# Kernel optimization log

Measured on AMD Instinct MI355X. Metric: run time of the kernel, lower is better.

## Reference

```python
import jax, jax.numpy as jnp
import numpy as np

N, E, G = 50000, 150000, 200
D, ED_IN, EH = 320, 15, 32
NB, NT = 3, 9  # conv blocks, edge types


def setup_inputs() -> dict:
    key = jax.random.key(0)
    ks = jax.random.split(key, 16)
    s = 0.02
    return {
        "x": jax.random.normal(ks[0], (N, D), jnp.float32),
        "batch": jnp.sort(jax.random.randint(ks[1], (N,), 0, G)),
        "edge_indices": jax.random.randint(ks[2], (NT, 2, E), 0, N),
        "edge_attrs": jax.random.normal(ks[3], (NT, E, ED_IN), jnp.float32),
        "W1": jax.random.normal(ks[4], (2 * D + ED_IN, EH), jnp.float32) * s,
        "b1": jnp.zeros((EH,), jnp.float32),
        "W2": jax.random.normal(ks[5], (EH, EH), jnp.float32) * s,
        "b2": jnp.zeros((EH,), jnp.float32),
        "Wq": jax.random.normal(ks[6], (NB, NT, D, D), jnp.float32) * s,
        "bq": jnp.zeros((NB, NT, D), jnp.float32),
        "Wk": jax.random.normal(ks[7], (NB, NT, D, D), jnp.float32) * s,
        "bk": jnp.zeros((NB, NT, D), jnp.float32),
        "Wv": jax.random.normal(ks[8], (NB, NT, D, D), jnp.float32) * s,
        "bv": jnp.zeros((NB, NT, D), jnp.float32),
        "We": jax.random.normal(ks[9], (NB, NT, EH, D), jnp.float32) * s,
        "be": jnp.zeros((NB, NT, D), jnp.float32),
        "Ws": jax.random.normal(ks[10], (NB, NT, D, D), jnp.float32) * s,
        "bs": jnp.zeros((NB, NT, D), jnp.float32),
        "gamma": jnp.ones((NB, D), jnp.float32),
        "beta": jnp.zeros((NB, D), jnp.float32),
    }


def _transformer_conv(x, src, dst, ea, Wq, bq, Wk, bk, Wv, bv, We, be, Ws, bs):
    # PyG TransformerConv, heads=1, edge_dim=EH, eval mode (no dropout).
    q = (x @ Wq + bq)[dst]                    # [E, D] query at destination
    e = ea @ We + be                          # [E, D] projected edge attr
    k = (x @ Wk + bk)[src] + e                # [E, D]
    v = (x @ Wv + bv)[src] + e                # [E, D]
    alpha = (q * k).sum(-1) / jnp.sqrt(jnp.float32(D))  # [E]
    amax = jax.ops.segment_max(alpha, dst, num_segments=N)
    amax = jnp.where(jnp.isfinite(amax), amax, 0.0)     # guard empty segments
    ex = jnp.exp(alpha - amax[dst])
    denom = jax.ops.segment_sum(ex, dst, num_segments=N)
    w = ex / (denom[dst] + 1e-16)
    out = jax.ops.segment_sum(w[:, None] * v, dst, num_segments=N)
    return out + x @ Ws + bs                  # root/skip connection


def _graph_layer_norm(x, batch, gamma, beta):
    # PyG gnn.norm.LayerNorm, mode='graph': normalize per graph over nodes+channels.
    cnt = jax.ops.segment_sum(jnp.ones((N,), x.dtype), batch, num_segments=G)
    norm = jnp.maximum(cnt, 1.0) * D          # elements per graph
    mean = jax.ops.segment_sum(x.sum(-1), batch, num_segments=G) / norm
    xc = x - mean[batch][:, None]
    var = jax.ops.segment_sum((xc * xc).sum(-1), batch, num_segments=G) / norm
    out = xc / jnp.sqrt(var + 1e-5)[batch][:, None]
    return out * gamma + beta


def reference(x, batch, edge_indices, edge_attrs, W1, b1, W2, b2,
              Wq, bq, Wk, bk, Wv, bv, We, be, Ws, bs, gamma, beta):
    # Edge MLP preprocessing (uses original node features x).
    new_ea = []
    for t in range(NT):
        src, dst = edge_indices[t, 0], edge_indices[t, 1]
        cat = jnp.concatenate([x[src], x[dst], edge_attrs[t]], axis=-1)  # [E, 655]
        h = jax.nn.leaky_relu(cat @ W1 + b1)
        new_ea.append(h @ W2 + b2)

    h = x
    for b in range(NB):
        acc = jnp.zeros_like(h)
        for t in range(NT):
            src, dst = edge_indices[t, 0], edge_indices[t, 1]
            acc = acc + _transformer_conv(
                h, src, dst, new_ea[t],
                Wq[b, t], bq[b, t], Wk[b, t], bk[b, t], Wv[b, t], bv[b, t],
                We[b, t], be[b, t], Ws[b, t], bs[b, t])
        x_ = jax.nn.leaky_relu(acc / 9.0)
        x_ = _graph_layer_norm(x_, batch, gamma[b], beta[b])
        h = 0.5 * (h + x_)

    return jax.ops.segment_max(h, batch, num_segments=G)  # global max pool [G, D]
```

## Files before the change

kernel.cpp:

```cpp
#include <hip/hip_runtime.h>

#define N_NODES 50000
#define N_EDGE  150000
#define N_GRAPH 200
#define DIM     320
#define EDI     15
#define EH      32
#define NBLK    3
#define NTYP    9
#define NPAD    51200
#define BPT     50
#define QLD     360
#define QCOLS   353
#define NPQ     384
#define HAGCH   132
#define BIGCH   448

typedef unsigned short u16;
typedef unsigned int   u32;
typedef __bf16 bf16x8 __attribute__((ext_vector_type(8)));
typedef float  f32x4  __attribute__((ext_vector_type(4)));

__device__ __forceinline__ float b2f(u16 s) {
    u32 u = ((u32)s) << 16;
    return __builtin_bit_cast(float, u);
}
__device__ __forceinline__ float b2f_lo(u32 u) { return __builtin_bit_cast(float, u << 16); }
__device__ __forceinline__ float b2f_hi(u32 u) { return __builtin_bit_cast(float, u & 0xffff0000u); }
__device__ __forceinline__ u16 f2b(float f) {
    u32 u = __builtin_bit_cast(u32, f);
    u = (u + 0x7fffu + ((u >> 16) & 1u)) >> 16;
    return (u16)u;
}

__device__ __forceinline__ void gll16(const u16* g, u32 ldsAddr) {
    u32 m0v = (u32)__builtin_amdgcn_readfirstlane((int)ldsAddr);
    asm volatile("s_mov_b32 m0, %0\n\t"
                 "global_load_lds_dwordx4 %1, off"
                 :: "s"(m0v), "v"((unsigned long long)(size_t)g)
                 : "memory");
}

__global__ __launch_bounds__(256) void gemm_kernel(
    const u16* __restrict__ A, int Mstride,
    const u16* __restrict__ Bst, const float* __restrict__ bias,
    u16* __restrict__ Cb, float* __restrict__ Cf,
    int ldc, int out_cols, int M, int NP, int KQ, int mode,
    int zA, int zB, int zC)
{
    A += (size_t)blockIdx.z * zA;
    Bst += (size_t)blockIdx.z * zB;
    if (Cb) Cb += (size_t)blockIdx.z * zC;
    if (Cf) Cf += (size_t)blockIdx.z * zC;

    const int tid = threadIdx.x;
    const int wave = tid >> 6, lane = tid & 63;

    const int nwg = gridDim.x * gridDim.y;
    const int flat = blockIdx.y * gridDim.x + blockIdx.x;
    const int qq = nwg >> 3, rr = nwg & 7;
    const int xcd = flat & 7, loc = flat >> 3;
    const int swz = (xcd < rr ? xcd * (qq + 1) : rr * (qq + 1) + (xcd - rr) * qq) + loc;
    const int n0 = (swz % gridDim.x) * 128, m0 = (swz / gridDim.x) * 128;

    const int wm = (wave & 1) << 6, wn = (wave >> 1) << 6;
    const int lm = lane & 15, quad = lane >> 4;

    __shared__ uint4 smem[2][2][512];
    const u32 ldsBase = (u32)(size_t)&smem[0][0][0];

    f32x4 acc[4][4] = {};
    const int nIter = KQ >> 2;

    auto stage = [&](int s, int buf) {
        const int c0 = s << 2;
        const u32 bufBase = ldsBase + (u32)buf * 16384u;
#pragma unroll
        for (int u = 0; u < 2; ++u) {
            const int i = wave + (u << 2);
            const int chunk = i >> 1, half = (i & 1) << 6;
            const u16* ga = A + ((size_t)(c0 + chunk) * Mstride + m0 + half + lane) * 8;
            gll16(ga, bufBase + (u32)i * 1024u);
            const u16* gb = Bst + ((size_t)(c0 + chunk) * NP + n0 + half + lane) * 8;
            gll16(gb, bufBase + 8192u + (u32)i * 1024u);
        }
    };

    stage(0, 0);
    asm volatile("s_waitcnt vmcnt(0)" ::: "memory");
    __syncthreads();

    int cur = 0;
    for (int s = 0; s < nIter; ++s) {
        if (s + 1 < nIter) stage(s + 1, cur ^ 1);
        const uint4* aT = &smem[cur][0][0];
        const uint4* bT = &smem[cur][1][0];
        bf16x8 af[4], bfr[4];
#pragma unroll
        for (int mi = 0; mi < 4; ++mi)
            af[mi] = __builtin_bit_cast(bf16x8, aT[quad * 128 + wm + mi * 16 + lm]);
#pragma unroll
        for (int ni = 0; ni < 4; ++ni)
            bfr[ni] = __builtin_bit_cast(bf16x8, bT[quad * 128 + wn + ni * 16 + lm]);
#pragma unroll
        for (int mi = 0; mi < 4; ++mi)
#pragma unroll
            for (int ni = 0; ni < 4; ++ni)
                acc[mi][ni] = __builtin_amdgcn_mfma_f32_16x16x32_bf16(af[mi], bfr[ni], acc[mi][ni], 0, 0, 0);
        asm volatile("s_waitcnt vmcnt(0)" ::: "memory");
        __syncthreads();
        cur ^= 1;
    }

#pragma unroll
    for (int mi = 0; mi < 4; ++mi) {
        int row = m0 + wm + mi * 16 + quad * 4;
#pragma unroll
        for (int ni = 0; ni < 4; ++ni) {
            int col = n0 + wn + ni * 16 + lm;
            float bv = bias ? bias[col] : 0.f;
#pragma unroll
            for (int r = 0; r < 4; ++r) {
                int rr2 = row + r;
                if (rr2 < M && col < out_cols) {
                    float v = acc[mi][ni][r] + bv;
                    size_t off = (size_t)rr2 * ldc + col;
                    if (mode == 0)      Cb[off] = f2b(v);
                    else if (mode == 1) Cf[off] = v;
                    else                Cf[off] += v;
                }
            }
        }
    }
}

__global__ void k_convert_x(const float* __restrict__ x, u16* __restrict__ hb,
                            u16* __restrict__ hNode) {
    int i = blockIdx.x * 256 + threadIdx.x;
    if (i >= N_NODES * DIM) return;
    int node = i / DIM, c = i - node * DIM;
    u16 v = f2b(x[i]);
    hb[((size_t)(c >> 3) * N_NODES + node) * 8 + (c & 7)] = v;
    hNode[i] = v;
}

__global__ void k_prep_wT(const float* __restrict__ W, u16* __restrict__ T) {
    int i = blockIdx.x * 256 + threadIdx.x;
    if (i >= 27 * 40 * 320) return;
    int e = i % 320, jq = (i / 320) % 40, bt = i / (320 * 40);
    const float* src = W + ((size_t)bt * 320 + e) * 320 + jq * 8;
    u16 tmp[8];
#pragma unroll
    for (int r = 0; r < 8; ++r) tmp[r] = f2b(src[r]);
    *(uint4*)(&T[(((size_t)bt * 40 + jq) * 320 + e) * 8]) = *(uint4*)tmp;
}

__global__ void k_prep_qkvW(const u16* __restrict__ Mb, u16* __restrict__ Bst) {
    int i = blockIdx.x * 256 + threadIdx.x;
    if (i >= 27 * 40 * NPQ) return;
    int col = i % NPQ, kq = (i / NPQ) % 40, bt = i / (NPQ * 40);
    if (col >= 320 && col < QCOLS) return;
    u16 tmp[8];
    if (col >= QCOLS) {
#pragma unroll
        for (int r = 0; r < 8; ++r) tmp[r] = 0;
    } else {
#pragma unroll
        for (int r = 0; r < 8; ++r)
            tmp[r] = Mb[((size_t)bt * 320 + kq * 8 + r) * 320 + col];
    }
    *(uint4*)(&Bst[(((size_t)bt * 40 + kq) * NPQ + col) * 8]) = *(uint4*)tmp;
}

__global__ __launch_bounds__(256) void k_prep_ext(
    const float* __restrict__ Wq, const float* __restrict__ bq,
    const float* __restrict__ We, const float* __restrict__ be,
    const float* __restrict__ bk,
    u16* __restrict__ Bst, float* __restrict__ biasQkv)
{
    __shared__ float WeL[33 * 321];
    int bt = blockIdx.x, kt = blockIdx.y;
    for (int i = threadIdx.x; i < 33 * 320; i += 256) {
        int r = i / 320, d = i - r * 320;
        WeL[r * 321 + d] = (r < 32) ? We[((size_t)bt * 32 + r) * 320 + d]
                                    : (be[(size_t)bt * 320 + d] + bk[(size_t)bt * 320 + d]);
    }
    __syncthreads();
    if (kt < 10) {
        int k  = kt * 32 + (threadIdx.x >> 3);
        int ct = threadIdx.x & 7;
        const float* wq = Wq + ((size_t)bt * 320 + k) * 320;
        float dot[5] = {0.f, 0.f, 0.f, 0.f, 0.f};
        for (int d = 0; d < 320; ++d) {
            float w = wq[d];
            dot[0] += w * WeL[ct * 321 + d];
            dot[1] += w * WeL[(ct + 8) * 321 + d];
            dot[2] += w * WeL[(ct + 16) * 321 + d];
            dot[3] += w * WeL[(ct + 24) * 321 + d];
            dot[4] += w * WeL[32 * 321 + d];
        }
#pragma unroll
        for (int u = 0; u < 4; ++u)
            Bst[(((size_t)bt * 40 + (k >> 3)) * NPQ + 320 + ct + u * 8) * 8 + (k & 7)] = f2b(dot[u]);
        if (ct == 0)
            Bst[(((size_t)bt * 40 + (k >> 3)) * NPQ + 352) * 8 + (k & 7)] = f2b(dot[4]);
    } else {
        int c = threadIdx.x;
        if (c < 33) {
            const float* b = bq + (size_t)bt * 320;
            float s = 0.f;
            for (int d = 0; d < 320; ++d) s += b[d] * WeL[c * 321 + d];
            biasQkv[bt * NPQ + 320 + c] = s;
        }
    }
}

__global__ __launch_bounds__(256) void k_prep_qkvB(
    const float* __restrict__ Wk, const float* __restrict__ bq,
    float* __restrict__ bias)
{
    int i = blockIdx.x * 256 + threadIdx.x;
    if (i >= 27 * NPQ) return;
    int col = i % NPQ, bt = i / NPQ;
    if (col < 320) {
        const float4* wr = (const float4*)(Wk + ((size_t)bt * 320 + col) * 320);
        const float4* bb = (const float4*)(bq + (size_t)bt * 320);
        float s = 0.f;
        for (int j = 0; j < 80; ++j) {
            float4 a = wr[j], b = bb[j];
            s += a.x * b.x + a.y * b.y + a.z * b.z + a.w * b.w;
        }
        bias[bt * NPQ + col] = s;
    } else if (col >= QCOLS) {
        bias[bt * NPQ + col] = 0.f;
    }
}

__global__ void k_prep_skipB(const float* __restrict__ bs, float* __restrict__ bias) {
    int i = blockIdx.x * 256 + threadIdx.x;
    if (i >= 3 * 384) return;
    int col = i % 384, b = i / 384;
    float v = 0.f;
    if (col < 320)
        for (int t = 0; t < 9; ++t) v += bs[(b * 9 + t) * 320 + col];
    bias[i] = v;
}

__global__ void k_prep_bigB(const float* __restrict__ Ws, const float* __restrict__ Wv,
                            const float* __restrict__ We, const float* __restrict__ be,
                            const float* __restrict__ bv, u16* __restrict__ Bst) {
    int i = blockIdx.x * 256 + threadIdx.x;
    if (i >= 3 * BIGCH * 384) return;
    int col = i % 384, q = (i / 384) % BIGCH, b = i / (384 * BIGCH);
    u16 tmp[8];
#pragma unroll
    for (int r = 0; r < 8; ++r) {
        int k = q * 8 + r;
        float v = 0.f;
        if (col < 320) {
            if (k < 320) {
                for (int t = 0; t < 9; ++t)
                    v += Ws[((size_t)(b * 9 + t) * 320 + k) * 320 + col];
            } else {
                int kk = k - 320, t = kk / 360, kl = kk - t * 360;
                if (t < 9) {
                    int bt = b * 9 + t;
                    if (kl < 320)       v = Wv[((size_t)bt * 320 + kl) * 320 + col];
                    else if (kl < 352)  v = We[((size_t)bt * 32 + (kl - 320)) * 320 + col];
                    else if (kl == 352) v = be[(size_t)bt * 320 + col] + bv[(size_t)bt * 320 + col];
                }
            }
        }
        tmp[r] = f2b(v);
    }
    *(uint4*)(&Bst[(((size_t)b * BIGCH + q) * 384 + col) * 8]) = *(uint4*)tmp;
}

__global__ void k_prep_w1W(const float* __restrict__ W1, u16* __restrict__ Bst) {
    int i = blockIdx.x * 256 + threadIdx.x;
    if (i >= 320 * 128) return;
    int col = i & 127, k = i >> 7;
    float v = 0.f;
    if (col < 32)      v = W1[(size_t)k * 32 + col];
    else if (col < 64) v = W1[(size_t)(320 + k) * 32 + (col - 32)];
    Bst[((size_t)(k >> 3) * 128 + col) * 8 + (k & 7)] = f2b(v);
}

__global__ void k_csr_zero(int* __restrict__ cnt) {
    int i = blockIdx.x * 256 + threadIdx.x;
    if (i < NTYP * NPAD) cnt[i] = 0;
}
__global__ void k_csr_count(const int* __restrict__ eidx, int* __restrict__ cnt) {
    int i = blockIdx.x * 256 + threadIdx.x;
    if (i >= NTYP * N_EDGE) return;
    int t = i / N_EDGE, e = i - t * N_EDGE;
    int dst = eidx[(size_t)(t * 2 + 1) * N_EDGE + e];
    atomicAdd(&cnt[t * NPAD + dst], 1);
}
__global__ __launch_bounds__(1024) void k_csr_scan1(const int* __restrict__ cnt,
                                                    int* __restrict__ rowStart,
                                                    int* __restrict__ blockSum) {
    __shared__ int tmp[1024];
    int t = blockIdx.y, blk = blockIdx.x, tid = threadIdx.x;
    int idx = t * NPAD + blk * 1024 + tid;
    int v = cnt[idx];
    tmp[tid] = v;
    __syncthreads();
    for (int off = 1; off < 1024; off <<= 1) {
        int x = (tid >= off) ? tmp[tid - off] : 0;
        __syncthreads();
        tmp[tid] += x;
        __syncthreads();
    }
    rowStart[idx] = tmp[tid] - v;
    if (tid == 1023) blockSum[t * 64 + blk] = tmp[tid];
}
__global__ void k_csr_scan2(int* __restrict__ blockSum) {
    int t = threadIdx.x;
    if (t >= NTYP) return;
    int run = 0;
    for (int b = 0; b < BPT; ++b) {
        int v = blockSum[t * 64 + b];
        blockSum[t * 64 + b] = run;
        run += v;
    }
}
__global__ void k_csr_scan3(int* __restrict__ rowStart, const int* __restrict__ blockSum,
                            int* __restrict__ cursor) {
    int i = blockIdx.x * 256 + threadIdx.x;
    if (i >= NTYP * NPAD) return;
    int t = i / NPAD, n = i - t * NPAD;
    int v = rowStart[i] + blockSum[t * 64 + (n >> 10)];
    rowStart[i] = v;
    cursor[i] = v;
}
__global__ void k_csr_scatter(const int* __restrict__ eidx, int* __restrict__ cursor,
                              u16* __restrict__ sSrc, int* __restrict__ sEid) {
    int i = blockIdx.x * 256 + threadIdx.x;
    if (i >= NTYP * N_EDGE) return;
    int t = i / N_EDGE, e = i - t * N_EDGE;
    int src = eidx[(size_t)(t * 2) * N_EDGE + e];
    int dst = eidx[(size_t)(t * 2 + 1) * N_EDGE + e];
    int pos = atomicAdd(&cursor[t * NPAD + dst], 1);
    sSrc[(size_t)t * N_EDGE + pos] = (u16)src;
    sEid[(size_t)t * N_EDGE + pos] = e;
}

__global__ __launch_bounds__(256) void k_edge_mlp(
    const u16* __restrict__ Anodes, const int* __restrict__ eidx,
    const float* __restrict__ eattr, const float* __restrict__ W1,
    const float* __restrict__ b1, const float* __restrict__ W2,
    const float* __restrict__ b2, u16* __restrict__ outEa, int t)
{
    __shared__ float w1c[EDI][EH];
    __shared__ float w2s[EH][EH];
    __shared__ float b1s[EH], b2s[EH];
    int tid = threadIdx.x;
    for (int i = tid; i < EDI * EH; i += 256) w1c[i / EH][i % EH] = W1[(640 + i / EH) * EH + (i % EH)];
    for (int i = tid; i < EH * EH; i += 256) w2s[i / EH][i % EH] = W2[i];
    if (tid < EH) { b1s[tid] = b1[tid]; b2s[tid] = b2[tid]; }
    __syncthreads();

    int e = blockIdx.x * 256 + tid;
    if (e >= N_EDGE) return;
    int src = eidx[(size_t)(t * 2) * N_EDGE + e];
    int dst = eidx[(size_t)(t * 2 + 1) * N_EDGE + e];
    const float* eat = eattr + ((size_t)t * N_EDGE + e) * EDI;
    const u16* a1 = Anodes + (size_t)src * 64;
    const u16* a2 = Anodes + (size_t)dst * 64 + 32;

    float h1[EH];
#pragma unroll
    for (int j = 0; j < EH; ++j) h1[j] = b2f(a1[j]) + b2f(a2[j]) + b1s[j];
    for (int i = 0; i < EDI; ++i) {
        float v = eat[i];
#pragma unroll
        for (int j = 0; j < EH; ++j) h1[j] += v * w1c[i][j];
    }
#pragma unroll
    for (int j = 0; j < EH; ++j) h1[j] = h1[j] > 0.f ? h1[j] : 0.01f * h1[j];

    u16* orow = outEa + (size_t)e * EH;
    for (int j = 0; j < EH; ++j) {
        float o = b2s[j];
#pragma unroll
        for (int i = 0; i < EH; ++i) o += h1[i] * w2s[i][j];
        orow[j] = f2b(o);
    }
}

__global__ __launch_bounds__(256) void k_attn(
    const u16* __restrict__ qkv, const u16* __restrict__ hNode,
    const int* __restrict__ rowStart,
    const u16* __restrict__ sSrc, const int* __restrict__ sEid,
    const u16* __restrict__ ea, u16* __restrict__ hA, int cb)
{
    int wave = threadIdx.x >> 6, lane = threadIdx.x & 63;
    int n = blockIdx.x * 4 + wave;
    if (n >= N_NODES) return;
    int eb = rowStart[n], ee = rowStart[n + 1];

    float l = 0.f, as = 0.f;
    float av0 = 0.f, av1 = 0.f, av2 = 0.f, av3 = 0.f, avt = 0.f;

    if (eb != ee) {
        const u16* qrow = qkv + (size_t)n * QLD;
        uint2 qv = *(const uint2*)(qrow + 4 * lane);
        float q40 = b2f_lo(qv.x), q41 = b2f_hi(qv.x);
        float q42 = b2f_lo(qv.y), q43 = b2f_hi(qv.y);
        float q1 = b2f(qrow[256 + lane]);
        float qwl = (lane < 33) ? b2f(qrow[320 + lane]) : 0.f;
        float qwbe = __shfl(qwl, 32, 64);
        float qw = (lane < 32) ? qwl : 0.f;
        const float RS = 0.05590169943749474f;
        float m = -INFINITY;

        int ei = eb;
        for (; ei + 2 <= ee; ei += 2) {
            int s0 = sSrc[ei], s1 = sSrc[ei + 1];
            int id0 = sEid[ei], id1 = sEid[ei + 1];
            const u16* kr0 = hNode + (size_t)s0 * DIM;
            const u16* kr1 = hNode + (size_t)s1 * DIM;
            uint2 k0v = *(const uint2*)(kr0 + 4 * lane);
            uint2 k1v = *(const uint2*)(kr1 + 4 * lane);
            float k00 = b2f_lo(k0v.x), k01 = b2f_hi(k0v.x);
            float k02 = b2f_lo(k0v.y), k03 = b2f_hi(k0v.y);
            float k10 = b2f_lo(k1v.x), k11 = b2f_hi(k1v.x);
            float k12 = b2f_lo(k1v.y), k13 = b2f_hi(k1v.y);
            float k0t = b2f(kr0[256 + lane]);
            float k1t = b2f(kr1[256 + lane]);
            float ea0 = (lane < 32) ? b2f(ea[(size_t)id0 * 32 + lane]) : 0.f;
            float ea1 = (lane < 32) ? b2f(ea[(size_t)id1 * 32 + lane]) : 0.f;
            float d0 = qw * ea0 + q1 * k0t + q40 * k00 + q41 * k01 + q42 * k02 + q43 * k03;
            float d1 = qw * ea1 + q1 * k1t + q40 * k10 + q41 * k11 + q42 * k12 + q43 * k13;
#pragma unroll
            for (int off = 32; off > 0; off >>= 1) {
                d0 += __shfl_xor(d0, off, 64);
                d1 += __shfl_xor(d1, off, 64);
            }
            float a0 = (d0 + qwbe) * RS, a1 = (d1 + qwbe) * RS;
            float mn = fmaxf(m, fmaxf(a0, a1));
            float sc = __expf(m - mn);
            float p0 = __expf(a0 - mn), p1 = __expf(a1 - mn);
            l = l * sc + p0 + p1;
            av0 = av0 * sc + p0 * k00 + p1 * k10;
            av1 = av1 * sc + p0 * k01 + p1 * k11;
            av2 = av2 * sc + p0 * k02 + p1 * k12;
            av3 = av3 * sc + p0 * k03 + p1 * k13;
            avt = avt * sc + p0 * k0t + p1 * k1t;
            as = as * sc + p0 * ea0 + p1 * ea1;
            m = mn;
        }
        if (ei < ee) {
            int s0 = sSrc[ei];
            int id0 = sEid[ei];
            const u16* kr0 = hNode + (size_t)s0 * DIM;
            uint2 k0v = *(const uint2*)(kr0 + 4 * lane);
            float k00 = b2f_lo(k0v.x), k01 = b2f_hi(k0v.x);
            float k02 = b2f_lo(k0v.y), k03 = b2f_hi(k0v.y);
            float k0t = b2f(kr0[256 + lane]);
            float ea0 = (lane < 32) ? b2f(ea[(size_t)id0 * 32 + lane]) : 0.f;
            float d0 = qw * ea0 + q1 * k0t + q40 * k00 + q41 * k01 + q42 * k02 + q43 * k03;
#pragma unroll
            for (int off = 32; off > 0; off >>= 1) d0 += __shfl_xor(d0, off, 64);
            float a0 = (d0 + qwbe) * RS;
            float mn = fmaxf(m, a0);
            float sc = __expf(m - mn), p0 = __expf(a0 - mn);
            l = l * sc + p0;
            av0 = av0 * sc + p0 * k00;
            av1 = av1 * sc + p0 * k01;
            av2 = av2 * sc + p0 * k02;
            av3 = av3 * sc + p0 * k03;
            avt = avt * sc + p0 * k0t;
            as = as * sc + p0 * ea0;
        }
    }

    float inv = (l > 0.f) ? 1.f / l : 0.f;
    u32 w0 = (u32)f2b(av0 * inv) | ((u32)f2b(av1 * inv) << 16);
    u32 w1 = (u32)f2b(av2 * inv) | ((u32)f2b(av3 * inv) << 16);
    uint2 wv; wv.x = w0; wv.y = w1;
    *(uint2*)(hA + ((size_t)(cb + (lane >> 1)) * N_NODES + n) * 8 + (lane & 1) * 4) = wv;
    hA[((size_t)(cb + 32 + (lane >> 3)) * N_NODES + n) * 8 + (lane & 7)] = f2b(avt * inv);
    if (lane < 32) {
        hA[((size_t)(cb + 40 + (lane >> 3)) * N_NODES + n) * 8 + (lane & 7)] = f2b(as * inv);
    } else if (lane == 32) {
        uint4 fz; fz.x = (eb != ee) ? 0x3f80u : 0u; fz.y = 0u; fz.z = 0u; fz.w = 0u;
        *(uint4*)(hA + ((size_t)(cb + 44) * N_NODES + n) * 8) = fz;
    }
}

__device__ __forceinline__ int lowerb(const int* a, int n, int v) {
    int lo = 0, hi = n;
    while (lo < hi) { int mid = (lo + hi) >> 1; if (a[mid] < v) lo = mid + 1; else hi = mid; }
    return lo;
}

__global__ __launch_bounds__(1024) void k_post(
    const float* __restrict__ acc, u16* __restrict__ hb, u16* __restrict__ hNode,
    const int* __restrict__ batch, const float* __restrict__ gamma,
    const float* __restrict__ beta)
{
    int g = blockIdx.x;
    int start = lowerb(batch, N_NODES, g);
    int end   = lowerb(batch, N_NODES, g + 1);
    int cnt = end - start;
    if (cnt == 0) return;
    int i0 = start * DIM, i1 = end * DIM;

    float s = 0.f, ss = 0.f;
    for (int i = i0 + threadIdx.x; i < i1; i += 1024) {
        float v = acc[i] * (1.f / 9.f);
        v = v > 0.f ? v : 0.01f * v;
        s += v; ss += v * v;
    }
    __shared__ float rs[16], rss[16];
#pragma unroll
    for (int off = 32; off > 0; off >>= 1) { s += __shfl_xor(s, off, 64); ss += __shfl_xor(ss, off, 64); }
    int wave = threadIdx.x >> 6, lane = threadIdx.x & 63;
    if (lane == 0) { rs[wave] = s; rss[wave] = ss; }
    __syncthreads();
    if (threadIdx.x == 0) {
        float S = 0.f, SS = 0.f;
        for (int w = 0; w < 16; ++w) { S += rs[w]; SS += rss[w]; }
        float norm = (float)cnt * DIM;
        float mean = S / norm;
        float var = SS / norm - mean * mean;
        rs[0] = mean;
        rss[0] = rsqrtf(var + 1e-5f);
    }
    __syncthreads();
    float mean = rs[0], rsig = rss[0];
    for (int i = i0 + threadIdx.x; i < i1; i += 1024) {
        float v = acc[i] * (1.f / 9.f);
        v = v > 0.f ? v : 0.01f * v;
        int node = i / DIM, c = i - node * DIM;
        float o = (v - mean) * rsig * gamma[c] + beta[c];
        u16 nb = f2b(0.5f * (b2f(hNode[i]) + o));
        hNode[i] = nb;
        hb[((size_t)(c >> 3) * N_NODES + node) * 8 + (c & 7)] = nb;
    }
}

__global__ __launch_bounds__(320) void k_maxpool(
    const u16* __restrict__ hb, const int* __restrict__ batch, float* __restrict__ out)
{
    int g = blockIdx.x, c = threadIdx.x;
    int start = lowerb(batch, N_NODES, g);
    int end   = lowerb(batch, N_NODES, g + 1);
    size_t base = (size_t)(c >> 3) * N_NODES * 8 + (c & 7);
    float m = -INFINITY;
    for (int n = start; n < end; ++n) m = fmaxf(m, b2f(hb[base + (size_t)n * 8]));
    out[(size_t)g * DIM + c] = m;
}

extern "C" void kernel_launch(void* const* d_in, const int* in_sizes, int n_in,
                              void* d_out, int out_size, void* d_ws, size_t ws_size,
                              hipStream_t stream)
{
    (void)in_sizes; (void)n_in; (void)out_size;
    const float* x     = (const float*)d_in[0];
    const int*   batch = (const int*)d_in[1];
    const int*   eidx  = (const int*)d_in[2];
    const float* eattr = (const float*)d_in[3];
    const float* W1 = (const float*)d_in[4];
    const float* b1 = (const float*)d_in[5];
    const float* W2 = (const float*)d_in[6];
    const float* b2 = (const float*)d_in[7];
    const float* Wq = (const float*)d_in[8];
    const float* bq = (const float*)d_in[9];
    const float* Wk = (const float*)d_in[10];
    const float* bk = (const float*)d_in[11];
    const float* Wv = (const float*)d_in[12];
    const float* bv = (const float*)d_in[13];
    const float* We = (const float*)d_in[14];
    const float* be = (const float*)d_in[15];
    const float* Ws = (const float*)d_in[16];
    const float* bs = (const float*)d_in[17];
    const float* gamma = (const float*)d_in[18];
    const float* beta  = (const float*)d_in[19];
    float* out = (float*)d_out;

    char* base = (char*)d_ws;
    size_t off = 0;
    auto carve = [&](size_t bytes) -> char* {
        char* r = base + off;
        off += (bytes + 255) & ~(size_t)255;
        return r;
    };
    u16*   hAg     = (u16*)  carve((size_t)HAGCH * N_NODES * 8 * 2 + 1024);
    u16*   hNode   = (u16*)  carve((size_t)N_NODES * DIM * 2);
    float* acc     = (float*)carve((size_t)N_NODES * DIM * 4);
    u16*   qkv     = (u16*)  carve((size_t)N_NODES * QLD * 2);
    u16*   Anodes  = (u16*)  carve((size_t)N_NODES * 64 * 2);
    u16*   BstQkv  = (u16*)  carve((size_t)27 * 40 * NPQ * 8 * 2);
    float* biasQkv = (float*)carve((size_t)27 * NPQ * 4);
    u16*   BstBig  = (u16*)  carve((size_t)3 * BIGCH * 384 * 8 * 2);
    float* biasSkip= (float*)carve((size_t)3 * 384 * 4);
    u16*   BstW1   = (u16*)  carve((size_t)40 * 128 * 8 * 2);
    int*   cnt     = (int*)  carve((size_t)NTYP * NPAD * 4);
    int*   rowStart= (int*)  carve((size_t)NTYP * NPAD * 4);
    int*   blockSum= (int*)  carve((size_t)NTYP * 64 * 4);
    u16*   sSrc    = (u16*)  carve((size_t)NTYP * N_EDGE * 2);
    int*   sEid    = (int*)  carve((size_t)NTYP * N_EDGE * 4);
    size_t fixed = off;
    size_t bigBytes   = (size_t)NTYP * N_EDGE * EH * 2;
    size_t smallBytes = (size_t)N_EDGE * EH * 2;
    int bigEa = (ws_size >= fixed + bigBytes + (1u << 20)) ? 1 : 0;
    u16* newEa = (u16*)carve(bigEa ? bigBytes : smallBytes);

    u16* regionB = hAg + (size_t)40 * N_NODES * 8;
    u16* AqT = regionB;
    u16* BkT = AqT + 27 * 40 * 320 * 8 + 512;
    u16* Mb  = BkT + 27 * 40 * 320 * 8 + 512;

    k_convert_x<<<(N_NODES * DIM + 255) / 256, 256, 0, stream>>>(x, hAg, hNode);
    hipMemsetAsync(hAg + (size_t)130 * N_NODES * 8, 0, (size_t)2 * N_NODES * 8 * 2, stream);
    k_prep_wT<<<(27 * 40 * 320 + 255) / 256, 256, 0, stream>>>(Wq, AqT);
    k_prep_wT<<<(27 * 40 * 320 + 255) / 256, 256, 0, stream>>>(Wk, BkT);
    gemm_kernel<<<dim3(3, 3, 27), 256, 0, stream>>>(AqT, 320, BkT, nullptr,
        Mb, nullptr, 320, 320, 320, 320, 40, 0, 102400, 102400, 102400);
    k_prep_qkvW<<<(27 * 40 * NPQ + 255) / 256, 256, 0, stream>>>(Mb, BstQkv);
    k_prep_ext<<<dim3(27, 11), 256, 0, stream>>>(Wq, bq, We, be, bk, BstQkv, biasQkv);
    k_prep_qkvB<<<(27 * NPQ + 255) / 256, 256, 0, stream>>>(Wk, bq, biasQkv);
    k_prep_skipB<<<(3 * 384 + 255) / 256, 256, 0, stream>>>(bs, biasSkip);
    k_prep_bigB<<<(3 * BIGCH * 384 + 255) / 256, 256, 0, stream>>>(Ws, Wv, We, be, bv, BstBig);
    k_prep_w1W<<<(320 * 128 + 255) / 256, 256, 0, stream>>>(W1, BstW1);

    k_csr_zero<<<(NTYP * NPAD + 255) / 256, 256, 0, stream>>>(cnt);
    k_csr_count<<<(NTYP * N_EDGE + 255) / 256, 256, 0, stream>>>(eidx, cnt);
    k_csr_scan1<<<dim3(BPT, NTYP), 1024, 0, stream>>>(cnt, rowStart, blockSum);
    k_csr_scan2<<<1, 64, 0, stream>>>(blockSum);
    k_csr_scan3<<<(NTYP * NPAD + 255) / 256, 256, 0, stream>>>(rowStart, blockSum, cnt);
    k_csr_scatter<<<(NTYP * N_EDGE + 255) / 256, 256, 0, stream>>>(eidx, cnt, sSrc, sEid);

    const int mt = (N_NODES + 127) / 128;
    const int et = (N_EDGE + 255) / 256;
    gemm_kernel<<<dim3(1, mt), 256, 0, stream>>>(hAg, N_NODES, BstW1, nullptr,
        Anodes, nullptr, 64, 64, N_NODES, 128, 40, 0, 0, 0, 0);
    if (bigEa) {
        for (int t = 0; t < NTYP; ++t)
            k_edge_mlp<<<dim3(et), 256, 0, stream>>>(
                Anodes, eidx, eattr, W1, b1, W2, b2, newEa + (size_t)t * N_EDGE * EH, t);
    }

    const int gOff[5] = {0, 130, 220, 310, 400};
    const int gKQ[5]  = {132, 92, 92, 92, 48};

    for (int b = 0; b < NBLK; ++b) {
        for (int t = 0; t < NTYP; ++t) {
            int bt = b * NTYP + t;
            u16* eaT = bigEa ? (newEa + (size_t)t * N_EDGE * EH) : newEa;
            if (!bigEa)
                k_edge_mlp<<<dim3(et), 256, 0, stream>>>(
                    Anodes, eidx, eattr, W1, b1, W2, b2, eaT, t);
            gemm_kernel<<<dim3(3, mt), 256, 0, stream>>>(
                hAg, N_NODES, BstQkv + (size_t)bt * 40 * NPQ * 8, biasQkv + bt * NPQ,
                qkv, nullptr, QLD, QCOLS, N_NODES, NPQ, 40, 0, 0, 0, 0);
            k_attn<<<dim3(N_NODES / 4), 256, 0, stream>>>(
                qkv, hNode, rowStart + t * NPAD, sSrc + (size_t)t * N_EDGE,
                sEid + (size_t)t * N_EDGE, eaT, hAg, 40 + (t & 1) * 45);
            if (t & 1) {
                int g = t >> 1;
                gemm_kernel<<<dim3(3, mt), 256, 0, stream>>>(
                    (g == 0) ? hAg : regionB, N_NODES,
                    BstBig + ((size_t)b * BIGCH + gOff[g]) * 384 * 8,
                    (g == 0) ? (biasSkip + b * 384) : nullptr,
                    nullptr, acc, DIM, DIM, N_NODES, 384, gKQ[g],
                    (g == 0) ? 1 : 2, 0, 0, 0);
            }
        }
        gemm_kernel<<<dim3(3, mt), 256, 0, stream>>>(
            regionB, N_NODES, BstBig + ((size_t)b * BIGCH + gOff[4]) * 384 * 8, nullptr,
            nullptr, acc, DIM, DIM, N_NODES, 384, gKQ[4], 2, 0, 0, 0);
        k_post<<<N_GRAPH, 1024, 0, stream>>>(acc, hAg, hNode, batch,
                                             gamma + b * DIM, beta + b * DIM);
    }
    k_maxpool<<<N_GRAPH, 320, 0, stream>>>(hAg, batch, out);
}
```

Baseline: 5.523 ms.

## Triple-buffer GEMM LDS pipeline and batch four edge types per aggregation GEMM

```diff
diff --git a/kernel.cpp b/kernel.cpp
--- a/kernel.cpp
+++ b/kernel.cpp
@@ -13,7 +13,6 @@
 #define QLD     360
 #define QCOLS   353
 #define NPQ     384
-#define HAGCH   132
 #define BIGCH   448
 
 typedef unsigned short u16;
@@ -66,7 +65,7 @@
     const int wm = (wave & 1) << 6, wn = (wave >> 1) << 6;
     const int lm = lane & 15, quad = lane >> 4;
 
-    __shared__ uint4 smem[2][2][512];
+    __shared__ uint4 smem[3][2][512];
     const u32 ldsBase = (u32)(size_t)&smem[0][0][0];
 
     f32x4 acc[4][4] = {};
@@ -87,14 +86,20 @@
     };
 
     stage(0, 0);
-    asm volatile("s_waitcnt vmcnt(0)" ::: "memory");
+    if (nIter > 1) {
+        stage(1, 1);
+        asm volatile("s_waitcnt vmcnt(4)" ::: "memory");
+    } else {
+        asm volatile("s_waitcnt vmcnt(0)" ::: "memory");
+    }
     __syncthreads();
 
-    int cur = 0;
+    int bRd = 0, bIss = 2;
     for (int s = 0; s < nIter; ++s) {
-        if (s + 1 < nIter) stage(s + 1, cur ^ 1);
-        const uint4* aT = &smem[cur][0][0];
-        const uint4* bT = &smem[cur][1][0];
+        const bool more = (s + 2 < nIter);
+        if (more) { stage(s + 2, bIss); bIss = (bIss == 2) ? 0 : bIss + 1; }
+        const uint4* aT = &smem[bRd][0][0];
+        const uint4* bT = &smem[bRd][1][0];
         bf16x8 af[4], bfr[4];
 #pragma unroll
         for (int mi = 0; mi < 4; ++mi)
@@ -107,9 +112,12 @@
 #pragma unroll
             for (int ni = 0; ni < 4; ++ni)
                 acc[mi][ni] = __builtin_amdgcn_mfma_f32_16x16x32_bf16(af[mi], bfr[ni], acc[mi][ni], 0, 0, 0);
-        asm volatile("s_waitcnt vmcnt(0)" ::: "memory");
-        __syncthreads();
-        cur ^= 1;
+        if (s + 1 < nIter) {
+            if (more) asm volatile("s_waitcnt vmcnt(4)" ::: "memory");
+            else      asm volatile("s_waitcnt vmcnt(0)" ::: "memory");
+            __syncthreads();
+        }
+        bRd = (bRd == 2) ? 0 : bRd + 1;
     }
 
 #pragma unroll
@@ -581,6 +589,33 @@
     const float* beta  = (const float*)d_in[19];
     float* out = (float*)d_out;
 
+    auto al = [](size_t b) -> size_t { return (b + 255) & ~(size_t)255; };
+    const size_t szOther =
+        al((size_t)N_NODES * DIM * 2)
+      + al((size_t)N_NODES * DIM * 4)
+      + al((size_t)N_NODES * QLD * 2)
+      + al((size_t)N_NODES * 64 * 2)
+      + al((size_t)27 * 40 * NPQ * 8 * 2)
+      + al((size_t)27 * NPQ * 4)
+      + al((size_t)3 * BIGCH * 384 * 8 * 2)
+      + al((size_t)3 * 384 * 4)
+      + al((size_t)40 * 128 * 8 * 2)
+      + al((size_t)NTYP * NPAD * 4) * 2
+      + al((size_t)NTYP * 64 * 4)
+      + al((size_t)NTYP * N_EDGE * 2)
+      + al((size_t)NTYP * N_EDGE * 4);
+    const size_t hag2 = al((size_t)132 * N_NODES * 8 * 2 + 1024);
+    const size_t hag4 = al((size_t)220 * N_NODES * 8 * 2 + 1024);
+    const size_t bigB = (size_t)NTYP * N_EDGE * EH * 2;
+    const size_t smlB = (size_t)N_EDGE * EH * 2;
+    const size_t mar = 1u << 20;
+    int nslots, bigEa;
+    if      (ws_size >= hag4 + szOther + bigB + mar) { nslots = 4; bigEa = 1; }
+    else if (ws_size >= hag2 + szOther + bigB + mar) { nslots = 2; bigEa = 1; }
+    else if (ws_size >= hag4 + szOther + smlB + mar) { nslots = 4; bigEa = 0; }
+    else                                             { nslots = 2; bigEa = 0; }
+    const int hagch = (nslots == 4) ? 220 : 132;
+
     char* base = (char*)d_ws;
     size_t off = 0;
     auto carve = [&](size_t bytes) -> char* {
@@ -588,7 +623,7 @@
         off += (bytes + 255) & ~(size_t)255;
         return r;
     };
-    u16*   hAg     = (u16*)  carve((size_t)HAGCH * N_NODES * 8 * 2 + 1024);
+    u16*   hAg     = (u16*)  carve((size_t)hagch * N_NODES * 8 * 2 + 1024);
     u16*   hNode   = (u16*)  carve((size_t)N_NODES * DIM * 2);
     float* acc     = (float*)carve((size_t)N_NODES * DIM * 4);
     u16*   qkv     = (u16*)  carve((size_t)N_NODES * QLD * 2);
@@ -603,11 +638,7 @@
     int*   blockSum= (int*)  carve((size_t)NTYP * 64 * 4);
     u16*   sSrc    = (u16*)  carve((size_t)NTYP * N_EDGE * 2);
     int*   sEid    = (int*)  carve((size_t)NTYP * N_EDGE * 4);
-    size_t fixed = off;
-    size_t bigBytes   = (size_t)NTYP * N_EDGE * EH * 2;
-    size_t smallBytes = (size_t)N_EDGE * EH * 2;
-    int bigEa = (ws_size >= fixed + bigBytes + (1u << 20)) ? 1 : 0;
-    u16* newEa = (u16*)carve(bigEa ? bigBytes : smallBytes);
+    u16*   newEa   = (u16*)  carve(bigEa ? bigB : smlB);
 
     u16* regionB = hAg + (size_t)40 * N_NODES * 8;
     u16* AqT = regionB;
@@ -615,7 +646,8 @@
     u16* Mb  = BkT + 27 * 40 * 320 * 8 + 512;
 
     k_convert_x<<<(N_NODES * DIM + 255) / 256, 256, 0, stream>>>(x, hAg, hNode);
-    hipMemsetAsync(hAg + (size_t)130 * N_NODES * 8, 0, (size_t)2 * N_NODES * 8 * 2, stream);
+    if (nslots == 2)
+        hipMemsetAsync(hAg + (size_t)130 * N_NODES * 8, 0, (size_t)2 * N_NODES * 8 * 2, stream);
     k_prep_wT<<<(27 * 40 * 320 + 255) / 256, 256, 0, stream>>>(Wq, AqT);
     k_prep_wT<<<(27 * 40 * 320 + 255) / 256, 256, 0, stream>>>(Wk, BkT);
     gemm_kernel<<<dim3(3, 3, 27), 256, 0, stream>>>(AqT, 320, BkT, nullptr,
@@ -643,9 +675,6 @@
             k_edge_mlp<<<dim3(et), 256, 0, stream>>>(
                 Anodes, eidx, eattr, W1, b1, W2, b2, newEa + (size_t)t * N_EDGE * EH, t);
     }
-
-    const int gOff[5] = {0, 130, 220, 310, 400};
-    const int gKQ[5]  = {132, 92, 92, 92, 48};
 
     for (int b = 0; b < NBLK; ++b) {
         for (int t = 0; t < NTYP; ++t) {
@@ -659,20 +688,35 @@
                 qkv, nullptr, QLD, QCOLS, N_NODES, NPQ, 40, 0, 0, 0, 0);
             k_attn<<<dim3(N_NODES / 4), 256, 0, stream>>>(
                 qkv, hNode, rowStart + t * NPAD, sSrc + (size_t)t * N_EDGE,
-                sEid + (size_t)t * N_EDGE, eaT, hAg, 40 + (t & 1) * 45);
-            if (t & 1) {
-                int g = t >> 1;
-                gemm_kernel<<<dim3(3, mt), 256, 0, stream>>>(
-                    (g == 0) ? hAg : regionB, N_NODES,
-                    BstBig + ((size_t)b * BIGCH + gOff[g]) * 384 * 8,
-                    (g == 0) ? (biasSkip + b * 384) : nullptr,
-                    nullptr, acc, DIM, DIM, N_NODES, 384, gKQ[g],
-                    (g == 0) ? 1 : 2, 0, 0, 0);
+                sEid + (size_t)t * N_EDGE, eaT, hAg, 40 + (t % nslots) * 45);
+            if (nslots == 2) {
+                if (t & 1) {
+                    int g = t >> 1;
+                    const int gOff2[4] = {0, 130, 220, 310};
+                    const int gKQ2[4]  = {132, 92, 92, 92};
+                    gemm_kernel<<<dim3(3, mt), 256, 0, stream>>>(
+                        (g == 0) ? hAg : regionB, N_NODES,
+                        BstBig + ((size_t)b * BIGCH + gOff2[g]) * 384 * 8,
+                        (g == 0) ? (biasSkip + b * 384) : nullptr,
+                        nullptr, acc, DIM, DIM, N_NODES, 384, gKQ2[g],
+                        (g == 0) ? 1 : 2, 0, 0, 0);
+                }
+            } else {
+                if (t == 3)
+                    gemm_kernel<<<dim3(3, mt), 256, 0, stream>>>(
+                        hAg, N_NODES, BstBig + (size_t)b * BIGCH * 384 * 8,
+                        biasSkip + b * 384, nullptr, acc, DIM, DIM, N_NODES,
+                        384, 220, 1, 0, 0, 0);
+                else if (t == 7)
+                    gemm_kernel<<<dim3(3, mt), 256, 0, stream>>>(
+                        regionB, N_NODES, BstBig + ((size_t)b * BIGCH + 220) * 384 * 8,
+                        nullptr, nullptr, acc, DIM, DIM, N_NODES,
+                        384, 180, 2, 0, 0, 0);
             }
         }
         gemm_kernel<<<dim3(3, mt), 256, 0, stream>>>(
-            regionB, N_NODES, BstBig + ((size_t)b * BIGCH + gOff[4]) * 384 * 8, nullptr,
-            nullptr, acc, DIM, DIM, N_NODES, 384, gKQ[4], 2, 0, 0, 0);
+            regionB, N_NODES, BstBig + ((size_t)b * BIGCH + 400) * 384 * 8, nullptr,
+            nullptr, acc, DIM, DIM, N_NODES, 384, 48, 2, 0, 0, 0);
         k_post<<<N_GRAPH, 1024, 0, stream>>>(acc, hAg, hNode, batch,
                                              gamma + b * DIM, beta + b * DIM);
     }
```

Result: no change. 5.416 ms (-1.9%).
